# Performance work log

Measured on AMD Instinct MI355X. Metric: run time of the kernel, lower is better.

## Reference

```python
import jax, jax.numpy as jnp
import numpy as np

NUM_HEADS = 4
GROUPS = 8
EPS = 1e-5


def group_norm(x, w, b):
    B, C, H, W = x.shape
    xg = x.reshape(B, GROUPS, C // GROUPS, H, W)
    mu = jnp.mean(xg, axis=(2, 3, 4), keepdims=True)
    var = jnp.var(xg, axis=(2, 3, 4), keepdims=True)
    xg = (xg - mu) * jax.lax.rsqrt(var + EPS)
    x = xg.reshape(B, C, H, W)
    return x * w[None, :, None, None] + b[None, :, None, None]


def setup_inputs() -> dict:
    key = jax.random.key(0)
    k1, k2, k3 = jax.random.split(key, 3)
    B, C, H, W = 16, 256, 32, 32
    x = jax.random.normal(k1, (B, C, H, W), dtype=jnp.float32)
    gn_w = jnp.ones((C,), dtype=jnp.float32)
    gn_b = jnp.zeros((C,), dtype=jnp.float32)
    qkv_w = jax.random.normal(k2, (3 * C, C), dtype=jnp.float32) * 0.02
    qkv_b = jnp.zeros((3 * C,), dtype=jnp.float32)
    proj_w = jax.random.normal(k3, (C, C), dtype=jnp.float32) * 0.02
    proj_b = jnp.zeros((C,), dtype=jnp.float32)
    return {"x": x, "gn_w": gn_w, "gn_b": gn_b, "qkv_w": qkv_w,
            "qkv_b": qkv_b, "proj_w": proj_w, "proj_b": proj_b}


def reference(x, gn_w, gn_b, qkv_w, qkv_b, proj_w, proj_b):
    B, C, H, W = x.shape
    Dh = C // NUM_HEADS
    N = H * W
    skip = x
    xn = group_norm(x, gn_w, gn_b)
    # 1x1 conv QKV projection: [B,3C,H,W]
    qkv = jnp.einsum('oc,bchw->bohw', qkv_w, xn) + qkv_b[None, :, None, None]
    # split channel dim 3C -> [3, heads, Dh], flatten spatial -> N
    qkv = qkv.reshape(B, 3, NUM_HEADS, Dh, N)
    qkv = jnp.transpose(qkv, (1, 0, 2, 4, 3))  # [3,B,heads,N,Dh]
    q, k, v = qkv[0], qkv[1], qkv[2]
    scale = 1.0 / np.sqrt(Dh).astype(np.float32)
    attn = jnp.einsum('bhnd,bhmd->bhnm', q, k) * scale  # [B,heads,N,N]
    attn = jax.nn.softmax(attn, axis=-1)
    out = jnp.einsum('bhnm,bhmd->bhnd', attn, v)  # [B,heads,N,Dh]
    out = jnp.transpose(out, (0, 1, 3, 2)).reshape(B, C, H, W)
    out = jnp.einsum('oc,bchw->bohw', proj_w, out) + proj_b[None, :, None, None]
    return out + skip
```

## Files before the change

### kernel.cpp

```cpp
#include <hip/hip_runtime.h>

typedef unsigned short u16;
typedef __bf16 bf16x8 __attribute__((ext_vector_type(8)));
typedef float f32x4 __attribute__((ext_vector_type(4)));

#define QSCALE 0.18033688011112042f

__device__ __forceinline__ u16 f2bf(float f) {
  __bf16 h = (__bf16)f;
  union { __bf16 b; u16 u; } cv;
  cv.b = h;
  return cv.u;
}
__device__ __forceinline__ unsigned pack2(float a, float b) {
#if __has_builtin(__builtin_amdgcn_cvt_pk_bf16_f32)
  typedef __bf16 bf16x2 __attribute__((ext_vector_type(2)));
  bf16x2 p = __builtin_amdgcn_cvt_pk_bf16_f32(a, b);
  union { bf16x2 v; unsigned u; } cv;
  cv.v = p;
  return cv.u;
#else
  return (unsigned)f2bf(a) | ((unsigned)f2bf(b) << 16);
#endif
}
__device__ __forceinline__ float fexp2(float x) {
  return __builtin_amdgcn_exp2f(x);
}
__device__ __forceinline__ void cp16(const u16* g, u16* l) {
  __builtin_amdgcn_global_load_lds(
      (const __attribute__((address_space(1))) void*)g,
      (__attribute__((address_space(3))) void*)l, 16, 0, 0);
}

__global__ __launch_bounds__(256) void prep(
    const float* __restrict__ qw, const float* __restrict__ pw,
    const float* __restrict__ x,
    u16* __restrict__ qwb, u16* __restrict__ pwb, float* __restrict__ stats) {
  __shared__ float sh1[256], sh2[256];
  const int blk = blockIdx.x;
  const int t = threadIdx.x;
  if (blk < 256) {
    int i = blk * 256 + t;
    const float* s; u16* d; int j;
    if (i < 49152) { s = qw; d = qwb; j = i; }
    else           { s = pw; d = pwb; j = i - 49152; }
    float4 v = *(const float4*)(s + (size_t)j * 4);
    uint2 o; o.x = pack2(v.x, v.y); o.y = pack2(v.z, v.w);
    *(uint2*)(d + (size_t)j * 4) = o;
    return;
  }
  const int bid = blk - 256;
  int cl = t >> 3;
  int off = (t & 7) * 4;
  const float* p = x + (size_t)bid * 32768 + (size_t)cl * 1024 + off;
  float s = 0.f, ss = 0.f;
#pragma unroll 8
  for (int i = 0; i < 32; ++i) {
    float4 v = *(const float4*)(p + i * 32);
    s += v.x + v.y + v.z + v.w;
    ss += v.x * v.x + v.y * v.y + v.z * v.z + v.w * v.w;
  }
  sh1[t] = s; sh2[t] = ss;
  __syncthreads();
  for (int st = 128; st > 0; st >>= 1) {
    if (t < st) { sh1[t] += sh1[t + st]; sh2[t] += sh2[t + st]; }
    __syncthreads();
  }
  if (t == 0) {
    float mean = sh1[0] * (1.f / 32768.f);
    float var = sh2[0] * (1.f / 32768.f) - mean * mean;
    stats[bid * 2] = mean;
    stats[bid * 2 + 1] = rsqrtf(var + 1e-5f);
  }
}

__global__ __launch_bounds__(256) void gemm_qkv(
    const u16* __restrict__ A, const float* __restrict__ x,
    const float* __restrict__ stats,
    const float* __restrict__ gw, const float* __restrict__ gb,
    const float* __restrict__ bias,
    u16* __restrict__ o_q, u16* __restrict__ o_k, u16* __restrict__ o_v) {
  const int l = blockIdx.x;
  const int xcd = l & 7;
  const int i2 = l >> 3;
  const int m_t = i2 % 6;
  const int nl6 = i2 / 6;
  const int nt = xcd * 16 + nl6;
  const int m0 = m_t * 128;
  const int n0 = nt * 128;
  const int b = nt >> 3;
  const int nsp0 = (nt & 7) * 128;

  const int t = threadIdx.x;
  const int wave = t >> 6, lane = t & 63, lm = lane & 15, quad = lane >> 4;
  const int wr = wave >> 1, wc = wave & 1;

  __shared__ u16 As[2][128 * 32];
  __shared__ u16 Bs[2][128 * 32];

  f32x4 acc[4][4];
  const f32x4 fzero = {0.f, 0.f, 0.f, 0.f};
#pragma unroll
  for (int i = 0; i < 4; ++i)
#pragma unroll
    for (int j = 0; j < 4; ++j) acc[i][j] = fzero;

  const int srow = t >> 2, scol = (t & 3) * 8;
  const u16* pA0 = A + (size_t)(m0 + srow) * 256 + scol;
  const u16* pA1 = A + (size_t)(m0 + 64 + srow) * 256 + scol;

  const int n2 = t & 63, gq = t >> 6;
  const float* xb = x + (size_t)b * 262144 + nsp0 + 2 * n2;
  const int gsw = (gq ^ (n2 & 3)) * 8;

  float2 vB[8];
  uint4 vA0, vA1;

#define LD_B(ki)                                                       \
  {                                                                    \
    const int cb = (ki) * 32 + gq * 8;                                 \
    _Pragma("unroll") for (int i = 0; i < 8; ++i)                      \
        vB[i] = *(const float2*)(xb + (size_t)(cb + i) * 1024);        \
  }
#define ST_B(ki, buf)                                                  \
  {                                                                    \
    const int cb = (ki) * 32 + gq * 8;                                 \
    const float mu = stats[(b * 8 + (ki)) * 2];                        \
    const float rq = stats[(b * 8 + (ki)) * 2 + 1];                    \
    float e0[8], e1[8];                                                \
    _Pragma("unroll") for (int i = 0; i < 8; ++i) {                    \
      const float w = gw[cb + i] * rq;                                 \
      const float bb = gb[cb + i] - mu * w;                            \
      e0[i] = vB[i].x * w + bb;                                        \
      e1[i] = vB[i].y * w + bb;                                        \
    }                                                                  \
    uint4 w0, w1;                                                      \
    w0.x = pack2(e0[0], e0[1]); w0.y = pack2(e0[2], e0[3]);            \
    w0.z = pack2(e0[4], e0[5]); w0.w = pack2(e0[6], e0[7]);            \
    w1.x = pack2(e1[0], e1[1]); w1.y = pack2(e1[2], e1[3]);            \
    w1.z = pack2(e1[4], e1[5]); w1.w = pack2(e1[6], e1[7]);            \
    *(uint4*)(Bs[buf] + (2 * n2) * 32 + gsw) = w0;                     \
    *(uint4*)(Bs[buf] + (2 * n2 + 1) * 32 + gsw) = w1;                 \
  }

  LD_B(0);
  vA0 = *(const uint4*)pA0;
  vA1 = *(const uint4*)pA1;
  ST_B(0, 0);
  *(uint4*)(As[0] + srow * 32 + scol) = vA0;
  *(uint4*)(As[0] + (64 + srow) * 32 + scol) = vA1;
  LD_B(1);
  vA0 = *(const uint4*)(pA0 + 32);
  vA1 = *(const uint4*)(pA1 + 32);

  for (int ki = 0; ki < 8; ++ki) {
    __syncthreads();
    if (ki + 1 < 8) {
      ST_B(ki + 1, (ki + 1) & 1);
      u16* as = As[(ki + 1) & 1];
      *(uint4*)(as + srow * 32 + scol) = vA0;
      *(uint4*)(as + (64 + srow) * 32 + scol) = vA1;
    }
    if (ki + 2 < 8) {
      LD_B(ki + 2);
      vA0 = *(const uint4*)(pA0 + (ki + 2) * 32);
      vA1 = *(const uint4*)(pA1 + (ki + 2) * 32);
    }
    const u16* as = As[ki & 1];
    const u16* bs = Bs[ki & 1];
    bf16x8 af[4], bf[4];
#pragma unroll
    for (int mb = 0; mb < 4; ++mb)
      af[mb] = *(const bf16x8*)(as + (wr * 64 + mb * 16 + lm) * 32 + quad * 8);
#pragma unroll
    for (int nb = 0; nb < 4; ++nb) {
      const int row = wc * 64 + nb * 16 + lm;
      bf[nb] = *(const bf16x8*)(bs + row * 32 + ((quad ^ ((row >> 1) & 3)) * 8));
    }
#pragma unroll
    for (int mb = 0; mb < 4; ++mb)
#pragma unroll
      for (int nb = 0; nb < 4; ++nb)
        acc[mb][nb] = __builtin_amdgcn_mfma_f32_16x16x32_bf16(af[mb], bf[nb],
                                                              acc[mb][nb], 0, 0, 0);
  }
#undef LD_B
#undef ST_B

#pragma unroll
  for (int mb = 0; mb < 4; ++mb) {
#pragma unroll
    for (int nb = 0; nb < 4; ++nb) {
      const int o = m0 + wr * 64 + mb * 16 + 4 * quad;
      const int ng = n0 + wc * 64 + nb * 16 + lm;
      const int bb = ng >> 10, n = ng & 1023;
      const int kind = o >> 8;
      const int h = (o >> 6) & 3;
      const int dd = o & 63;
      const int jc = n >> 6, jl = n & 63;
      const size_t bhoff = ((size_t)(bb * 4 + h)) * 65536 + jc * 4096;
      if (kind <= 1) {
        const float sc = (kind == 0) ? QSCALE : 1.f;
        u16* base = (kind == 0) ? o_q : o_k;
        ushort4 pq;
        pq.x = f2bf((acc[mb][nb][0] + bias[o]) * sc);
        pq.y = f2bf((acc[mb][nb][1] + bias[o + 1]) * sc);
        pq.z = f2bf((acc[mb][nb][2] + bias[o + 2]) * sc);
        pq.w = f2bf((acc[mb][nb][3] + bias[o + 3]) * sc);
        *(ushort4*)(base + bhoff + jl * 64 + (((dd >> 3) ^ (jl & 7)) * 8) +
                    (dd & 7)) = pq;
      } else {
        u16* vbase = o_v + bhoff + (jl & 7);
#pragma unroll
        for (int r = 0; r < 4; ++r) {
          const int d = dd + r;
          vbase[d * 64 + (((jl >> 3) ^ (d & 7)) * 8)] =
              f2bf(acc[mb][nb][r] + bias[o + r]);
        }
      }
    }
  }
}

__global__ __launch_bounds__(256) void gemm_proj(
    const u16* __restrict__ A, const u16* __restrict__ Bm,
    const float* __restrict__ bias,
    const float* __restrict__ skip, float* __restrict__ out) {
  const int m0 = blockIdx.y * 64;
  const int n0 = blockIdx.x * 128;
  const int t = threadIdx.x;
  const int wave = t >> 6, lane = t & 63, lm = lane & 15, quad = lane >> 4;
  const int wr = wave >> 1, wc = wave & 1;

  __shared__ u16 As[2][64 * 32];
  __shared__ u16 Bs[2][128 * 32];

  f32x4 acc[2][4];
  const f32x4 fzero = {0.f, 0.f, 0.f, 0.f};
#pragma unroll
  for (int i = 0; i < 2; ++i)
#pragma unroll
    for (int j = 0; j < 4; ++j) acc[i][j] = fzero;

  const int srow = t >> 2, scol = (t & 3) * 8;
  const u16* pA0 = A + (size_t)(m0 + srow) * 256 + scol;
  const u16* pB0 = Bm + (size_t)(n0 + srow) * 256 + scol;
  const u16* pB1 = Bm + (size_t)(n0 + 64 + srow) * 256 + scol;

  uint4 pa0 = *(const uint4*)pA0;
  uint4 pb0 = *(const uint4*)pB0;
  uint4 pb1 = *(const uint4*)pB1;
  *(uint4*)(As[0] + srow * 32 + scol) = pa0;
  *(uint4*)(Bs[0] + srow * 32 + scol) = pb0;
  *(uint4*)(Bs[0] + (64 + srow) * 32 + scol) = pb1;
  pa0 = *(const uint4*)(pA0 + 32);
  pb0 = *(const uint4*)(pB0 + 32);
  pb1 = *(const uint4*)(pB1 + 32);

  for (int ki = 0; ki < 8; ++ki) {
    __syncthreads();
    if (ki + 1 < 8) {
      u16* as = As[(ki + 1) & 1];
      u16* bs = Bs[(ki + 1) & 1];
      *(uint4*)(as + srow * 32 + scol) = pa0;
      *(uint4*)(bs + srow * 32 + scol) = pb0;
      *(uint4*)(bs + (64 + srow) * 32 + scol) = pb1;
    }
    if (ki + 2 < 8) {
      const int ko = (ki + 2) * 32;
      pa0 = *(const uint4*)(pA0 + ko);
      pb0 = *(const uint4*)(pB0 + ko);
      pb1 = *(const uint4*)(pB1 + ko);
    }
    const u16* as = As[ki & 1];
    const u16* bs = Bs[ki & 1];
    bf16x8 af[2], bf[4];
#pragma unroll
    for (int mb = 0; mb < 2; ++mb)
      af[mb] = *(const bf16x8*)(as + (wr * 32 + mb * 16 + lm) * 32 + quad * 8);
#pragma unroll
    for (int nb = 0; nb < 4; ++nb)
      bf[nb] = *(const bf16x8*)(bs + (wc * 64 + nb * 16 + lm) * 32 + quad * 8);
#pragma unroll
    for (int mb = 0; mb < 2; ++mb)
#pragma unroll
      for (int nb = 0; nb < 4; ++nb)
        acc[mb][nb] = __builtin_amdgcn_mfma_f32_16x16x32_bf16(af[mb], bf[nb],
                                                              acc[mb][nb], 0, 0, 0);
  }

#pragma unroll
  for (int mb = 0; mb < 2; ++mb) {
#pragma unroll
    for (int nb = 0; nb < 4; ++nb) {
      const int o = m0 + wr * 32 + mb * 16 + 4 * quad;
      const int ng = n0 + wc * 64 + nb * 16 + lm;
      const int b = ng >> 10, n = ng & 1023;
#pragma unroll
      for (int r = 0; r < 4; ++r) {
        const size_t oi = ((size_t)(b * 256 + o + r)) * 1024 + n;
        out[oi] = acc[mb][nb][r] + bias[o + r] + skip[oi];
      }
    }
  }
}

__global__ __launch_bounds__(256) void attn_fused(
    const u16* __restrict__ qsw, const u16* __restrict__ ksw,
    const u16* __restrict__ vsw, u16* __restrict__ att) {
  const int bid = blockIdx.x;
  const int bh = (bid & 7) * 8 + ((bid >> 3) & 7);
  const int qtile = bid >> 6;
  const int t = threadIdx.x;
  const int wave = t >> 6, lane = t & 63, lm = lane & 15, quad = lane >> 4;

  const u16* qb = qsw + (size_t)bh * 65536 + qtile * 4096;
  const u16* kb = ksw + (size_t)bh * 65536;
  const u16* vb = vsw + (size_t)bh * 65536;

  __shared__ u16 KV[2][2][4096];
  __shared__ u16 QP[4096];

  const int t8 = t * 8;

  cp16(qb + t8, QP + t8);
  cp16(qb + 2048 + t8, QP + 2048 + t8);
  cp16(kb + t8, KV[0][0] + t8);
  cp16(kb + 2048 + t8, KV[0][0] + 2048 + t8);
  cp16(vb + t8, KV[0][1] + t8);
  cp16(vb + 2048 + t8, KV[0][1] + 2048 + t8);
  __syncthreads();

  const int swz0 = (quad ^ (lm & 7)) * 8;
  const int swz1 = ((4 + quad) ^ (lm & 7)) * 8;
  u16* Pw = QP + (wave * 16 + lm) * 64;
  const bf16x8 qf0 = *(const bf16x8*)(Pw + swz0);
  const bf16x8 qf1 = *(const bf16x8*)(Pw + swz1);

  const f32x4 fzero = {0.f, 0.f, 0.f, 0.f};
  f32x4 oacc[4];
#pragma unroll
  for (int d = 0; d < 4; ++d) oacc[d] = fzero;
  float lp = 0.f;

  for (int jc = 0; jc < 16; ++jc) {
    if (jc) __syncthreads();
    if (jc + 1 < 16) {
      const int base = (jc + 1) * 4096;
      u16* kd = KV[(jc + 1) & 1][0];
      u16* vd = KV[(jc + 1) & 1][1];
      cp16(kb + base + t8, kd + t8);
      cp16(kb + base + 2048 + t8, kd + 2048 + t8);
      cp16(vb + base + t8, vd + t8);
      cp16(vb + base + 2048 + t8, vd + 2048 + t8);
    }
    const u16* Ks = KV[jc & 1][0];
    const u16* Vs = KV[jc & 1][1];

    f32x4 sacc[4];
#pragma unroll
    for (int jb = 0; jb < 4; ++jb) sacc[jb] = fzero;
#pragma unroll
    for (int jb = 0; jb < 4; ++jb) {
      const int row = (jb * 16 + lm) * 64;
      bf16x8 kf0 = *(const bf16x8*)(Ks + row + swz0);
      bf16x8 kf1 = *(const bf16x8*)(Ks + row + swz1);
      sacc[jb] = __builtin_amdgcn_mfma_f32_16x16x32_bf16(kf0, qf0, sacc[jb], 0, 0, 0);
      sacc[jb] = __builtin_amdgcn_mfma_f32_16x16x32_bf16(kf1, qf1, sacc[jb], 0, 0, 0);
    }
#pragma unroll
    for (int jb = 0; jb < 4; ++jb) {
      const float e0 = fexp2(sacc[jb][0]);
      const float e1_ = fexp2(sacc[jb][1]);
      const float e2 = fexp2(sacc[jb][2]);
      const float e3 = fexp2(sacc[jb][3]);
      lp += (e0 + e1_) + (e2 + e3);
      uint2 pw;
      pw.x = pack2(e0, e1_);
      pw.y = pack2(e2, e3);
      const int oct = 2 * jb + (quad >> 1);
      *(uint2*)(Pw + ((oct ^ (lm & 7)) * 8) + 4 * (quad & 1)) = pw;
    }
    bf16x8 pf0 = *(const bf16x8*)(Pw + swz0);
    bf16x8 pf1 = *(const bf16x8*)(Pw + swz1);
#pragma unroll
    for (int db = 0; db < 4; ++db) {
      const int row = (db * 16 + lm) * 64;
      bf16x8 vf0 = *(const bf16x8*)(Vs + row + swz0);
      bf16x8 vf1 = *(const bf16x8*)(Vs + row + swz1);
      oacc[db] = __builtin_amdgcn_mfma_f32_16x16x32_bf16(pf0, vf0, oacc[db], 0, 0, 0);
      oacc[db] = __builtin_amdgcn_mfma_f32_16x16x32_bf16(pf1, vf1, oacc[db], 0, 0, 0);
    }
  }

  float rs = lp;
  rs += __shfl_xor(rs, 16);
  rs += __shfl_xor(rs, 32);
  const int b = bh >> 2, h = bh & 3;
#pragma unroll
  for (int r = 0; r < 4; ++r) {
    const float inv = 1.f / __shfl(rs, 4 * quad + r);
    const int n = qtile * 64 + wave * 16 + 4 * quad + r;
#pragma unroll
    for (int db = 0; db < 4; ++db) {
      const int c = h * 64 + db * 16 + lm;
      att[((size_t)(b * 1024 + n)) * 256 + c] = f2bf(oacc[db][r] * inv);
    }
  }
}

extern "C" void kernel_launch(void* const* d_in, const int* in_sizes, int n_in,
                              void* d_out, int out_size, void* d_ws, size_t ws_size,
                              hipStream_t stream) {
  const float* x      = (const float*)d_in[0];
  const float* gn_w   = (const float*)d_in[1];
  const float* gn_b   = (const float*)d_in[2];
  const float* qkv_w  = (const float*)d_in[3];
  const float* qkv_b  = (const float*)d_in[4];
  const float* proj_w = (const float*)d_in[5];
  const float* proj_b = (const float*)d_in[6];
  float* out = (float*)d_out;

  char* ws = (char*)d_ws;
  float* stats = (float*)(ws + 0);
  u16* qwb = (u16*)(ws + 4096);
  u16* pwb = (u16*)(ws + 397312);
  u16* qsw = (u16*)(ws + 8916992);
  u16* ksw = (u16*)(ws + 17305600);
  u16* vsw = (u16*)(ws + 25694208);
  u16* att = (u16*)(ws + 34082816);

  prep<<<384, 256, 0, stream>>>(qkv_w, proj_w, x, qwb, pwb, stats);
  gemm_qkv<<<768, 256, 0, stream>>>(qwb, x, stats, gn_w, gn_b, qkv_b,
                                    qsw, ksw, vsw);
  attn_fused<<<1024, 256, 0, stream>>>(qsw, ksw, vsw, att);
  gemm_proj<<<dim3(128, 4), 256, 0, stream>>>(pwb, att, proj_b, x, out);
}
```

Baseline: 138.9 us.

## Switch attention to 32x32x16 MFMA with key-split waves and LDS reduction

The fused attention kernel moves from 16x16x32 to 32x32x16 bf16 MFMA. Each wave now takes a 32-query block and one half of every 64-key chunk, instead of 16 queries over the full chunk. The two key halves are combined at the end through an LDS reduction, and the output is written as 4-element vector stores. The aim is fewer MFMA issues and fewer LDS fragment loads per unit of work, at the cost of an extra barrier plus the reduction, and larger accumulator register use.

```diff
diff --git a/kernel.cpp b/kernel.cpp
--- a/kernel.cpp
+++ b/kernel.cpp
@@ -3,6 +3,7 @@
 typedef unsigned short u16;
 typedef __bf16 bf16x8 __attribute__((ext_vector_type(8)));
 typedef float f32x4 __attribute__((ext_vector_type(4)));
+typedef float f32x16 __attribute__((ext_vector_type(16)));
 
 #define QSCALE 0.18033688011112042f
 
@@ -312,7 +313,9 @@
   const int bh = (bid & 7) * 8 + ((bid >> 3) & 7);
   const int qtile = bid >> 6;
   const int t = threadIdx.x;
-  const int wave = t >> 6, lane = t & 63, lm = lane & 15, quad = lane >> 4;
+  const int wave = t >> 6, lane = t & 63;
+  const int l5 = lane & 31, h = lane >> 5;
+  const int iblk = wave & 1, jh = wave >> 1;
 
   const u16* qb = qsw + (size_t)bh * 65536 + qtile * 4096;
   const u16* kb = ksw + (size_t)bh * 65536;
@@ -322,7 +325,6 @@
   __shared__ u16 QP[4096];
 
   const int t8 = t * 8;
-
   cp16(qb + t8, QP + t8);
   cp16(qb + 2048 + t8, QP + 2048 + t8);
   cp16(kb + t8, KV[0][0] + t8);
@@ -331,16 +333,19 @@
   cp16(vb + 2048 + t8, KV[0][1] + 2048 + t8);
   __syncthreads();
 
-  const int swz0 = (quad ^ (lm & 7)) * 8;
-  const int swz1 = ((4 + quad) ^ (lm & 7)) * 8;
-  u16* Pw = QP + (wave * 16 + lm) * 64;
-  const bf16x8 qf0 = *(const bf16x8*)(Pw + swz0);
-  const bf16x8 qf1 = *(const bf16x8*)(Pw + swz1);
-
-  const f32x4 fzero = {0.f, 0.f, 0.f, 0.f};
-  f32x4 oacc[4];
-#pragma unroll
-  for (int d = 0; d < 4; ++d) oacc[d] = fzero;
+  const int qrow = iblk * 32 + l5;
+  bf16x8 qf[4];
+#pragma unroll
+  for (int sd = 0; sd < 4; ++sd)
+    qf[sd] = *(const bf16x8*)(QP + qrow * 64 + (((2 * sd + h) ^ (qrow & 7)) * 8));
+  __syncthreads();
+
+  u16* Pw = QP + wave * 1024;
+  const int pswz = (l5 >> 1) & 3;
+
+  f32x16 oacc0, oacc1;
+#pragma unroll
+  for (int r = 0; r < 16; ++r) { oacc0[r] = 0.f; oacc1[r] = 0.f; }
   float lp = 0.f;
 
   for (int jc = 0; jc < 16; ++jc) {
@@ -357,54 +362,77 @@
     const u16* Ks = KV[jc & 1][0];
     const u16* Vs = KV[jc & 1][1];
 
-    f32x4 sacc[4];
-#pragma unroll
-    for (int jb = 0; jb < 4; ++jb) sacc[jb] = fzero;
-#pragma unroll
-    for (int jb = 0; jb < 4; ++jb) {
-      const int row = (jb * 16 + lm) * 64;
-      bf16x8 kf0 = *(const bf16x8*)(Ks + row + swz0);
-      bf16x8 kf1 = *(const bf16x8*)(Ks + row + swz1);
-      sacc[jb] = __builtin_amdgcn_mfma_f32_16x16x32_bf16(kf0, qf0, sacc[jb], 0, 0, 0);
-      sacc[jb] = __builtin_amdgcn_mfma_f32_16x16x32_bf16(kf1, qf1, sacc[jb], 0, 0, 0);
-    }
-#pragma unroll
-    for (int jb = 0; jb < 4; ++jb) {
-      const float e0 = fexp2(sacc[jb][0]);
-      const float e1_ = fexp2(sacc[jb][1]);
-      const float e2 = fexp2(sacc[jb][2]);
-      const float e3 = fexp2(sacc[jb][3]);
-      lp += (e0 + e1_) + (e2 + e3);
+    f32x16 sacc;
+#pragma unroll
+    for (int r = 0; r < 16; ++r) sacc[r] = 0.f;
+    const int krow = jh * 32 + l5;
+    const int kswz = krow & 7;
+#pragma unroll
+    for (int sd = 0; sd < 4; ++sd) {
+      bf16x8 kf = *(const bf16x8*)(Ks + krow * 64 + (((2 * sd + h) ^ kswz) * 8));
+      sacc = __builtin_amdgcn_mfma_f32_32x32x16_bf16(kf, qf[sd], sacc, 0, 0, 0);
+    }
+#pragma unroll
+    for (int g = 0; g < 4; ++g) {
+      const float e0 = fexp2(sacc[4 * g + 0]);
+      const float e1 = fexp2(sacc[4 * g + 1]);
+      const float e2 = fexp2(sacc[4 * g + 2]);
+      const float e3 = fexp2(sacc[4 * g + 3]);
+      lp += (e0 + e1) + (e2 + e3);
       uint2 pw;
-      pw.x = pack2(e0, e1_);
+      pw.x = pack2(e0, e1);
       pw.y = pack2(e2, e3);
-      const int oct = 2 * jb + (quad >> 1);
-      *(uint2*)(Pw + ((oct ^ (lm & 7)) * 8) + 4 * (quad & 1)) = pw;
-    }
-    bf16x8 pf0 = *(const bf16x8*)(Pw + swz0);
-    bf16x8 pf1 = *(const bf16x8*)(Pw + swz1);
-#pragma unroll
-    for (int db = 0; db < 4; ++db) {
-      const int row = (db * 16 + lm) * 64;
-      bf16x8 vf0 = *(const bf16x8*)(Vs + row + swz0);
-      bf16x8 vf1 = *(const bf16x8*)(Vs + row + swz1);
-      oacc[db] = __builtin_amdgcn_mfma_f32_16x16x32_bf16(pf0, vf0, oacc[db], 0, 0, 0);
-      oacc[db] = __builtin_amdgcn_mfma_f32_16x16x32_bf16(pf1, vf1, oacc[db], 0, 0, 0);
-    }
-  }
-
-  float rs = lp;
-  rs += __shfl_xor(rs, 16);
-  rs += __shfl_xor(rs, 32);
-  const int b = bh >> 2, h = bh & 3;
-#pragma unroll
-  for (int r = 0; r < 4; ++r) {
-    const float inv = 1.f / __shfl(rs, 4 * quad + r);
-    const int n = qtile * 64 + wave * 16 + 4 * quad + r;
-#pragma unroll
-    for (int db = 0; db < 4; ++db) {
-      const int c = h * 64 + db * 16 + lm;
-      att[((size_t)(b * 1024 + n)) * 256 + c] = f2bf(oacc[db][r] * inv);
+      *(uint2*)(Pw + l5 * 32 + ((g ^ pswz) * 8) + 4 * h) = pw;
+    }
+    bf16x8 pf[2];
+#pragma unroll
+    for (int sj = 0; sj < 2; ++sj)
+      pf[sj] = *(const bf16x8*)(Pw + l5 * 32 + (((2 * sj + h) ^ pswz) * 8));
+#pragma unroll
+    for (int sj = 0; sj < 2; ++sj) {
+      const int vrow0 = l5;
+      const int vrow1 = 32 + l5;
+      const int gv = 4 * jh + 2 * sj + h;
+      bf16x8 vf0 = *(const bf16x8*)(Vs + vrow0 * 64 + ((gv ^ (vrow0 & 7)) * 8));
+      bf16x8 vf1 = *(const bf16x8*)(Vs + vrow1 * 64 + ((gv ^ (vrow1 & 7)) * 8));
+      oacc0 = __builtin_amdgcn_mfma_f32_32x32x16_bf16(vf0, pf[sj], oacc0, 0, 0, 0);
+      oacc1 = __builtin_amdgcn_mfma_f32_32x32x16_bf16(vf1, pf[sj], oacc1, 0, 0, 0);
+    }
+  }
+
+  lp += __shfl_xor(lp, 32);
+
+  float* cb = (float*)KV[0];
+  __syncthreads();
+  if (jh == 1) {
+    float* d = cb + (iblk * 64 + lane) * 33;
+#pragma unroll
+    for (int r = 0; r < 16; ++r) { d[r] = oacc0[r]; d[16 + r] = oacc1[r]; }
+    d[32] = lp;
+  }
+  __syncthreads();
+  if (jh == 0) {
+    const float* s = cb + (iblk * 64 + lane) * 33;
+#pragma unroll
+    for (int r = 0; r < 16; ++r) { oacc0[r] += s[r]; oacc1[r] += s[16 + r]; }
+    lp += s[32];
+    const float inv = 1.f / lp;
+    const int b = bh >> 2, hh = bh & 3;
+    const int n = qtile * 64 + iblk * 32 + l5;
+    u16* obase = att + ((size_t)(b * 1024 + n)) * 256 + hh * 64;
+#pragma unroll
+    for (int g = 0; g < 4; ++g) {
+      ushort4 o0, o1;
+      o0.x = f2bf(oacc0[4 * g + 0] * inv);
+      o0.y = f2bf(oacc0[4 * g + 1] * inv);
+      o0.z = f2bf(oacc0[4 * g + 2] * inv);
+      o0.w = f2bf(oacc0[4 * g + 3] * inv);
+      o1.x = f2bf(oacc1[4 * g + 0] * inv);
+      o1.y = f2bf(oacc1[4 * g + 1] * inv);
+      o1.z = f2bf(oacc1[4 * g + 2] * inv);
+      o1.w = f2bf(oacc1[4 * g + 3] * inv);
+      *(ushort4*)(obase + 8 * g + 4 * h) = o0;
+      *(ushort4*)(obase + 32 + 8 * g + 4 * h) = o1;
     }
   }
 }
```

New measurement: 139.0 us (median of 2 runs). Within noise of the previous version (+0.1%).
